# Kernel tuning notes

Hardware: AMD Instinct MI355X
Metric: run time of the kernel (lower is better)

Reference implementation:

```python
import jax, jax.numpy as jnp
import numpy as np

H = 1.0  # binarization scale (default in module)

def round_through(x):
    # straight-through estimator: forward = round(x), backward = identity
    return x + jax.lax.stop_gradient(jnp.round(x) - x)

def binary_tanh_unit(x):
    hs = jnp.clip((x + 1.0) / 2.0, 0.0, 1.0)  # hard sigmoid
    return 2.0 * round_through(hs) - 1.0

def setup_inputs() -> dict:
    key = jax.random.key(0)
    kx, kw, kb = jax.random.split(key, 3)
    N, d_in, d_out = 16384, 1024, 1024
    x = jax.random.normal(kx, (N, d_in), dtype=jnp.float32)
    # kernel initialized uniform in [-H, H] per the module
    W = jax.random.uniform(kw, (d_in, d_out), dtype=jnp.float32, minval=-H, maxval=H)
    b = jax.random.normal(kb, (d_out,), dtype=jnp.float32) * 0.01
    return {"x": x, "W": W, "b": b}

def reference(x, W, b):
    # binarize weights to +/-H, then dense matmul + bias
    Wb = H * binary_tanh_unit(W / H)  # values in {-H, +H}
    out = jnp.matmul(x, Wb) + b       # [N, d_out]
    return out
```

## Files before the change

### kernel.cpp

```cpp
#include <hip/hip_runtime.h>
#include <stdint.h>

typedef __bf16 bf16_t;
typedef __bf16 bf16x8 __attribute__((ext_vector_type(8)));
typedef float f32x4 __attribute__((ext_vector_type(4)));

#define M_DIM 16384
#define N_DIM 1024
#define K_DIM 1024
#define BM 128
#define BN 256
#define BK 32
#define NT (K_DIM / BK)
#define A_SLOT 8192
#define B_SLOT 16384
#define B_BASE 16384

__global__ void bin_transpose_w(const float* __restrict__ W,
                                unsigned short* __restrict__ WbT) {
    __shared__ unsigned short t[64][68];
    int tj = blockIdx.x;
    int ti = blockIdx.y;
    int tid = threadIdx.x;
    int c4 = (tid & 15) * 4;
    int r0 = tid >> 4;
#pragma unroll
    for (int p = 0; p < 4; ++p) {
        int r = r0 + p * 16;
        float4 v = *(const float4*)(W + (size_t)(ti * 64 + r) * N_DIM + tj * 64 + c4);
        t[r][c4 + 0] = ((v.x + 1.0f) * 0.5f > 0.5f) ? 0x3F80 : 0xBF80;
        t[r][c4 + 1] = ((v.y + 1.0f) * 0.5f > 0.5f) ? 0x3F80 : 0xBF80;
        t[r][c4 + 2] = ((v.z + 1.0f) * 0.5f > 0.5f) ? 0x3F80 : 0xBF80;
        t[r][c4 + 3] = ((v.w + 1.0f) * 0.5f > 0.5f) ? 0x3F80 : 0xBF80;
    }
    __syncthreads();
#pragma unroll
    for (int p = 0; p < 4; ++p) {
        int rn = r0 + p * 16;
        ushort4 o;
        o.x = t[c4 + 0][rn];
        o.y = t[c4 + 1][rn];
        o.z = t[c4 + 2][rn];
        o.w = t[c4 + 3][rn];
        *(ushort4*)(WbT + (size_t)(tj * 64 + rn) * K_DIM + ti * 64 + c4) = o;
    }
}

__device__ __forceinline__ void gload16(const void* g, const void* l) {
    __builtin_amdgcn_global_load_lds(
        (const __attribute__((address_space(1))) void*)(g),
        (__attribute__((address_space(3))) void*)(l),
        16, 0, 0);
}

__global__ __launch_bounds__(512, 4) void bgemm(const float* __restrict__ X,
                                                const bf16_t* __restrict__ Bt,
                                                const float* __restrict__ bias,
                                                float* __restrict__ C) {
    __shared__ __align__(16) char lds[2 * A_SLOT + 2 * B_SLOT];

    const int nwg = (M_DIM / BM) * (N_DIM / BN);
    int bid = blockIdx.x;
    int swz = (bid & 7) * (nwg >> 3) + (bid >> 3);
    int tile_n = swz & 3;
    int tile_m = swz >> 2;
    int bm0 = tile_m * BM;
    int bn0 = tile_n * BN;

    int tid = threadIdx.x;
    int w = tid >> 6, l = tid & 63;
    int wr = w >> 2, wc = w & 3;
    int lr = l & 15, lk = l >> 4;

    int ar = tid >> 2, ac = tid & 3;
    int aslot = ac ^ ((ar >> 1) & 3);
    const float* asrc = X + (size_t)(bm0 + ar) * K_DIM + ac * 8;

    int brow = tid >> 2;
    int bchk = (tid & 3) ^ ((brow >> 1) & 3);
    auto stageB = [&](int t, int c) {
        gload16(Bt + (size_t)(bn0 + c * 128 + brow) * K_DIM + t * BK + bchk * 8,
                lds + B_BASE + (t & 1) * B_SLOT + c * 8192 + tid * 16);
    };
    auto writeA = [&](int t, float4 lo, float4 hi) {
        bf16x8 v;
        v[0] = (__bf16)lo.x; v[1] = (__bf16)lo.y;
        v[2] = (__bf16)lo.z; v[3] = (__bf16)lo.w;
        v[4] = (__bf16)hi.x; v[5] = (__bf16)hi.y;
        v[6] = (__bf16)hi.z; v[7] = (__bf16)hi.w;
        *(bf16x8*)(lds + (t & 1) * A_SLOT + ar * 64 + aslot * 16) = v;
    };

    f32x4 acc[4][4];
#pragma unroll
    for (int m = 0; m < 4; ++m)
#pragma unroll
        for (int n = 0; n < 4; ++n)
            acc[m][n] = (f32x4)(0.0f);

    float4 aL0, aH0, aL1, aH1;

    { const float4* s = (const float4*)(asrc + 0 * BK); aL0 = s[0]; aH0 = s[1]; }
    stageB(0, 0); stageB(0, 1);
    { const float4* s = (const float4*)(asrc + 1 * BK); aL1 = s[0]; aH1 = s[1]; }
    writeA(0, aL0, aH0);
    asm volatile("s_waitcnt vmcnt(2)" ::: "memory");
    asm volatile("s_waitcnt lgkmcnt(0)" ::: "memory");
    __builtin_amdgcn_s_barrier();

#define TILE_BODY(T, CUR_L, CUR_H, NXT_L, NXT_H)                                  \
    {                                                                             \
        const int t_ = (T);                                                       \
        if (t_ + 1 < NT) { stageB(t_ + 1, 0); stageB(t_ + 1, 1); }                \
        if (t_ + 2 < NT) {                                                        \
            const float4* s = (const float4*)(asrc + (t_ + 2) * BK);              \
            CUR_L = s[0]; CUR_H = s[1];                   \
        }                                                                         \
        const char* Ab = lds + (t_ & 1) * A_SLOT;                                 \
        const char* Bb = lds + B_BASE + (t_ & 1) * B_SLOT;                        \
        bf16x8 bfr[4];                                                            \
        _Pragma("unroll") for (int n = 0; n < 4; ++n) {                           \
            int br = wc * 64 + n * 16 + lr;                                       \
            bfr[n] = *(const bf16x8*)(Bb + br * 64 + ((lk ^ ((br >> 1) & 3)) * 16)); \
        }                                                                         \
        _Pragma("unroll") for (int m = 0; m < 4; ++m) {                           \
            int r = wr * 64 + m * 16 + lr;                                        \
            bf16x8 afr = *(const bf16x8*)(Ab + r * 64 + ((lk ^ ((r >> 1) & 3)) * 16)); \
            _Pragma("unroll") for (int n = 0; n < 4; ++n)                         \
                acc[m][n] = __builtin_amdgcn_mfma_f32_16x16x32_bf16(              \
                    afr, bfr[n], acc[m][n], 0, 0, 0);                             \
        }                                                                         \
        if (t_ + 1 < NT) {                                                        \
            writeA(t_ + 1, NXT_L, NXT_H);        \
            if (t_ + 2 < NT)                                                      \
                asm volatile("s_waitcnt vmcnt(2)" ::: "memory");   \
            else                                                                  \
                asm volatile("s_waitcnt vmcnt(0)" ::: "memory");                  \
            asm volatile("s_waitcnt lgkmcnt(0)" ::: "memory");                    \
            __builtin_amdgcn_s_barrier();                                         \
        }                                                                         \
    }

    for (int tt = 0; tt < NT; tt += 2) {
        TILE_BODY(tt,     aL0, aH0, aL1, aH1);
        TILE_BODY(tt + 1, aL1, aH1, aL0, aH0);
    }
#undef TILE_BODY

#pragma unroll
    for (int n = 0; n < 4; ++n) {
        int col = bn0 + wc * 64 + n * 16 + lr;
        float bv = bias[col];
#pragma unroll
        for (int m = 0; m < 4; ++m) {
            int row0 = bm0 + wr * 64 + m * 16 + lk * 4;
#pragma unroll
            for (int j = 0; j < 4; ++j)
                C[(size_t)(row0 + j) * N_DIM + col] = acc[m][n][j] + bv;
        }
    }
}

__global__ void naive_bin_dense(const float* __restrict__ x,
                                const float* __restrict__ W,
                                const float* __restrict__ b,
                                float* __restrict__ out) {
    int col = blockIdx.x * 256 + threadIdx.x;
    int row = blockIdx.y;
    float acc = 0.0f;
    for (int k = 0; k < K_DIM; ++k) {
        float s = ((W[(size_t)k * N_DIM + col] + 1.0f) * 0.5f > 0.5f) ? 1.0f : -1.0f;
        acc += x[(size_t)row * K_DIM + k] * s;
    }
    out[(size_t)row * N_DIM + col] = acc + b[col];
}

extern "C" void kernel_launch(void* const* d_in, const int* in_sizes, int n_in,
                              void* d_out, int out_size, void* d_ws, size_t ws_size,
                              hipStream_t stream) {
    const float* x = (const float*)d_in[0];
    const float* W = (const float*)d_in[1];
    const float* b = (const float*)d_in[2];
    float* out = (float*)d_out;

    size_t wb_bytes = (size_t)K_DIM * N_DIM * sizeof(unsigned short);

    if (ws_size >= wb_bytes) {
        unsigned short* wbt = (unsigned short*)d_ws;
        hipLaunchKernelGGL(bin_transpose_w, dim3(N_DIM / 64, K_DIM / 64), dim3(256),
                           0, stream, W, wbt);
        hipLaunchKernelGGL(bgemm, dim3((M_DIM / BM) * (N_DIM / BN)), dim3(512), 0, stream,
                           x, (const bf16_t*)wbt, b, out);
    } else {
        hipLaunchKernelGGL(naive_bin_dense, dim3(N_DIM / 256, M_DIM), dim3(256),
                           0, stream, x, W, b, out);
    }
}
```

Before: 49.47 us.

## Shrink GEMM tile to 128x128 with 256 threads and raise MFMA priority

Changes the workgroup tile from 128x256 with 512 threads to 128x128 with 256 threads. Each thread now loads and converts two rows of the fp32 X tile, and the B staging, wave layout and swizzle are adjusted to match. It also wraps the MFMA block in s_setprio so matrix work gets scheduling priority. The smaller tile doubles the number of workgroups and may raise occupancy, but each X tile is now read from global memory by twice as many workgroups, which adds fp32 traffic and conversion work.

```diff
diff --git a/kernel.cpp b/kernel.cpp
--- a/kernel.cpp
+++ b/kernel.cpp
@@ -9,11 +9,11 @@
 #define N_DIM 1024
 #define K_DIM 1024
 #define BM 128
-#define BN 256
+#define BN 128
 #define BK 32
 #define NT (K_DIM / BK)
 #define A_SLOT 8192
-#define B_SLOT 16384
+#define B_SLOT 8192
 #define B_BASE 16384
 
 __global__ void bin_transpose_w(const float* __restrict__ W,
@@ -53,7 +53,7 @@
         16, 0, 0);
 }
 
-__global__ __launch_bounds__(512, 4) void bgemm(const float* __restrict__ X,
+__global__ __launch_bounds__(256, 4) void bgemm(const float* __restrict__ X,
                                                 const bf16_t* __restrict__ Bt,
                                                 const float* __restrict__ bias,
                                                 float* __restrict__ C) {
@@ -62,33 +62,42 @@
     const int nwg = (M_DIM / BM) * (N_DIM / BN);
     int bid = blockIdx.x;
     int swz = (bid & 7) * (nwg >> 3) + (bid >> 3);
-    int tile_n = swz & 3;
-    int tile_m = swz >> 2;
+    int tile_n = swz & 7;
+    int tile_m = swz >> 3;
     int bm0 = tile_m * BM;
     int bn0 = tile_n * BN;
 
     int tid = threadIdx.x;
     int w = tid >> 6, l = tid & 63;
-    int wr = w >> 2, wc = w & 3;
+    int wr = w >> 1, wc = w & 1;
     int lr = l & 15, lk = l >> 4;
 
     int ar = tid >> 2, ac = tid & 3;
-    int aslot = ac ^ ((ar >> 1) & 3);
-    const float* asrc = X + (size_t)(bm0 + ar) * K_DIM + ac * 8;
-
-    int brow = tid >> 2;
-    int bchk = (tid & 3) ^ ((brow >> 1) & 3);
+    int aslot1 = ac ^ ((ar >> 1) & 3);
+    int aslot2 = ac ^ (((ar + 64) >> 1) & 3);
+    const float* asrc1 = X + (size_t)(bm0 + ar) * K_DIM + ac * 8;
+    const float* asrc2 = asrc1 + (size_t)64 * K_DIM;
+
+    int brow0 = tid >> 2;
     auto stageB = [&](int t, int c) {
-        gload16(Bt + (size_t)(bn0 + c * 128 + brow) * K_DIM + t * BK + bchk * 8,
-                lds + B_BASE + (t & 1) * B_SLOT + c * 8192 + tid * 16);
+        int brow = c * 64 + brow0;
+        int bchk = (tid & 3) ^ ((brow >> 1) & 3);
+        gload16(Bt + (size_t)(bn0 + brow) * K_DIM + t * BK + bchk * 8,
+                lds + B_BASE + (t & 1) * B_SLOT + c * 4096 + tid * 16);
     };
-    auto writeA = [&](int t, float4 lo, float4 hi) {
+    auto writeA = [&](int t, float4 p0, float4 p1, float4 q0, float4 q1) {
         bf16x8 v;
-        v[0] = (__bf16)lo.x; v[1] = (__bf16)lo.y;
-        v[2] = (__bf16)lo.z; v[3] = (__bf16)lo.w;
-        v[4] = (__bf16)hi.x; v[5] = (__bf16)hi.y;
-        v[6] = (__bf16)hi.z; v[7] = (__bf16)hi.w;
-        *(bf16x8*)(lds + (t & 1) * A_SLOT + ar * 64 + aslot * 16) = v;
+        v[0] = (__bf16)p0.x; v[1] = (__bf16)p0.y;
+        v[2] = (__bf16)p0.z; v[3] = (__bf16)p0.w;
+        v[4] = (__bf16)p1.x; v[5] = (__bf16)p1.y;
+        v[6] = (__bf16)p1.z; v[7] = (__bf16)p1.w;
+        *(bf16x8*)(lds + (t & 1) * A_SLOT + ar * 64 + aslot1 * 16) = v;
+        bf16x8 u;
+        u[0] = (__bf16)q0.x; u[1] = (__bf16)q0.y;
+        u[2] = (__bf16)q0.z; u[3] = (__bf16)q0.w;
+        u[4] = (__bf16)q1.x; u[5] = (__bf16)q1.y;
+        u[6] = (__bf16)q1.z; u[7] = (__bf16)q1.w;
+        *(bf16x8*)(lds + (t & 1) * A_SLOT + (ar + 64) * 64 + aslot2 * 16) = u;
     };
 
     f32x4 acc[4][4];
@@ -98,23 +107,29 @@
         for (int n = 0; n < 4; ++n)
             acc[m][n] = (f32x4)(0.0f);
 
-    float4 aL0, aH0, aL1, aH1;
-
-    { const float4* s = (const float4*)(asrc + 0 * BK); aL0 = s[0]; aH0 = s[1]; }
+    float4 p00, p01, q00, q01;
+    float4 p10, p11, q10, q11;
+
+    { const float4* s1 = (const float4*)(asrc1 + 0 * BK);
+      const float4* s2 = (const float4*)(asrc2 + 0 * BK);
+      p00 = s1[0]; p01 = s1[1]; q00 = s2[0]; q01 = s2[1]; }
     stageB(0, 0); stageB(0, 1);
-    { const float4* s = (const float4*)(asrc + 1 * BK); aL1 = s[0]; aH1 = s[1]; }
-    writeA(0, aL0, aH0);
-    asm volatile("s_waitcnt vmcnt(2)" ::: "memory");
+    { const float4* s1 = (const float4*)(asrc1 + 1 * BK);
+      const float4* s2 = (const float4*)(asrc2 + 1 * BK);
+      p10 = s1[0]; p11 = s1[1]; q10 = s2[0]; q11 = s2[1]; }
+    writeA(0, p00, p01, q00, q01);
+    asm volatile("s_waitcnt vmcnt(4)" ::: "memory");
     asm volatile("s_waitcnt lgkmcnt(0)" ::: "memory");
     __builtin_amdgcn_s_barrier();
 
-#define TILE_BODY(T, CUR_L, CUR_H, NXT_L, NXT_H)                                  \
+#define TILE_BODY(T, CP0, CP1, CQ0, CQ1, NP0, NP1, NQ0, NQ1)                      \
     {                                                                             \
         const int t_ = (T);                                                       \
         if (t_ + 1 < NT) { stageB(t_ + 1, 0); stageB(t_ + 1, 1); }                \
         if (t_ + 2 < NT) {                                                        \
-            const float4* s = (const float4*)(asrc + (t_ + 2) * BK);              \
-            CUR_L = s[0]; CUR_H = s[1];                   \
+            const float4* s1 = (const float4*)(asrc1 + (t_ + 2) * BK);            \
+            const float4* s2 = (const float4*)(asrc2 + (t_ + 2) * BK);            \
+            CP0 = s1[0]; CP1 = s1[1]; CQ0 = s2[0]; CQ1 = s2[1];                   \
         }                                                                         \
         const char* Ab = lds + (t_ & 1) * A_SLOT;                                 \
         const char* Bb = lds + B_BASE + (t_ & 1) * B_SLOT;                        \
@@ -123,6 +138,7 @@
             int br = wc * 64 + n * 16 + lr;                                       \
             bfr[n] = *(const bf16x8*)(Bb + br * 64 + ((lk ^ ((br >> 1) & 3)) * 16)); \
         }                                                                         \
+        __builtin_amdgcn_s_setprio(1);                                            \
         _Pragma("unroll") for (int m = 0; m < 4; ++m) {                           \
             int r = wr * 64 + m * 16 + lr;                                        \
             bf16x8 afr = *(const bf16x8*)(Ab + r * 64 + ((lk ^ ((r >> 1) & 3)) * 16)); \
@@ -130,10 +146,11 @@
                 acc[m][n] = __builtin_amdgcn_mfma_f32_16x16x32_bf16(              \
                     afr, bfr[n], acc[m][n], 0, 0, 0);                             \
         }                                                                         \
+        __builtin_amdgcn_s_setprio(0);                                            \
         if (t_ + 1 < NT) {                                                        \
-            writeA(t_ + 1, NXT_L, NXT_H);        \
+            writeA(t_ + 1, NP0, NP1, NQ0, NQ1);     \
             if (t_ + 2 < NT)                                                      \
-                asm volatile("s_waitcnt vmcnt(2)" ::: "memory");   \
+                asm volatile("s_waitcnt vmcnt(4)" ::: "memory");   \
             else                                                                  \
                 asm volatile("s_waitcnt vmcnt(0)" ::: "memory");                  \
             asm volatile("s_waitcnt lgkmcnt(0)" ::: "memory");                    \
@@ -142,8 +159,8 @@
     }
 
     for (int tt = 0; tt < NT; tt += 2) {
-        TILE_BODY(tt,     aL0, aH0, aL1, aH1);
-        TILE_BODY(tt + 1, aL1, aH1, aL0, aH0);
+        TILE_BODY(tt,     p00, p01, q00, q01, p10, p11, q10, q11);
+        TILE_BODY(tt + 1, p10, p11, q10, q11, p00, p01, q00, q01);
     }
 #undef TILE_BODY
 
@@ -189,7 +206,7 @@
         unsigned short* wbt = (unsigned short*)d_ws;
         hipLaunchKernelGGL(bin_transpose_w, dim3(N_DIM / 64, K_DIM / 64), dim3(256),
                            0, stream, W, wbt);
-        hipLaunchKernelGGL(bgemm, dim3((M_DIM / BM) * (N_DIM / BN)), dim3(512), 0, stream,
+        hipLaunchKernelGGL(bgemm, dim3((M_DIM / BM) * (N_DIM / BN)), dim3(256), 0, stream,
                            x, (const bf16_t*)wbt, b, out);
     } else {
         hipLaunchKernelGGL(naive_bin_dense, dim3(N_DIM / 256, M_DIM), dim3(256),
```

Measured after the change: 60.24 us. 1.22x slower.
